# Optimization experiments

Measured on AMD Instinct MI355X. Metric: run time of the kernel, lower is better.

The kernel has to match this reference:

```python
import jax, jax.numpy as jnp
import numpy as np

B, T, D, H = 4096, 200, 128, 128


def setup_inputs() -> dict:
    key = jax.random.key(0)
    ks = jax.random.split(key, 9)
    s = 1.0 / np.sqrt(D + H)  # torch Linear default init bound
    u = lambda k, shape: jax.random.uniform(k, shape, jnp.float32, -s, s)
    return {
        "inputs": jax.random.normal(ks[0], (B, T, D), jnp.float32),
        "attention_scores": jax.random.uniform(ks[1], (B, T), jnp.float32),
        "h0": jnp.zeros((B, H), jnp.float32),
        "Wz": u(ks[2], (D + H, H)), "bz": u(ks[3], (H,)),
        "Wr": u(ks[4], (D + H, H)), "br": u(ks[5], (H,)),
        "Wh": u(ks[6], (D + H, H)), "bh": u(ks[7], (H,)),
    }


def reference(inputs, attention_scores, h0, Wz, bz, Wr, br, Wh, bh):
    # AUGRU: GRU with attention-modulated update gate (DIEN Sec 3.3).
    def step(h, xs):
        x_t, a_t = xs  # [B,D], [B]
        comb = jnp.concatenate([x_t, h], axis=-1)            # [B, D+H]
        z = jax.nn.sigmoid(comb @ Wz + bz)                   # [B, H]
        r = jax.nn.sigmoid(comb @ Wr + br)                   # [B, H]
        comb_r = jnp.concatenate([x_t, r * h], axis=-1)      # [B, D+H]
        h_tilde = jnp.tanh(comb_r @ Wh + bh)                 # [B, H]
        zp = a_t[:, None] * z                                # attention-scaled update gate
        h_new = (1.0 - zp) * h + zp * h_tilde
        return h_new, None

    xs = (jnp.swapaxes(inputs, 0, 1),            # [T, B, D]
          jnp.swapaxes(attention_scores, 0, 1))  # [T, B]
    h_final, _ = jax.lax.scan(step, h0, xs)
    return h_final  # [B, H]
```

## Files before the change

kernel.cpp:

```cpp
#include <hip/hip_runtime.h>
#include <stdint.h>

#define BB 4096
#define TT 200
#define DD 128
#define HH 128

typedef __attribute__((ext_vector_type(8))) short bf16x8;
typedef __attribute__((ext_vector_type(4))) float f32x4;

__device__ __forceinline__ short f2bf(float f) {
    uint32_t u = __builtin_bit_cast(uint32_t, f);
    u += 0x7fffu + ((u >> 16) & 1u);
    return (short)(u >> 16);
}
__device__ __forceinline__ uint32_t pk2(float a, float b) {
    uint32_t r;
    asm("v_cvt_pk_bf16_f32 %0, %1, %2" : "=v"(r) : "v"(a), "v"(b));
    return r;
}
__device__ __forceinline__ float sigm(float x) {
    return __builtin_amdgcn_rcpf(1.0f + __expf(-x));
}
__device__ __forceinline__ float tanhf_(float x) {
    return 2.0f * __builtin_amdgcn_rcpf(1.0f + __expf(-2.0f * x)) - 1.0f;
}
__device__ __forceinline__ void bar_lds() {
    asm volatile("s_waitcnt lgkmcnt(0)" ::: "memory");
    __builtin_amdgcn_sched_barrier(0);
    __builtin_amdgcn_s_barrier();
    __builtin_amdgcn_sched_barrier(0);
}


#define STEP(T, XR0, XR1) { \
    const int sn_ = ((T) + 1) & 1; \
    *(uint4*)&xbuf[sn_][xrow][xg_swz] = \
        make_uint4(pk2(XR0.x, XR0.y), pk2(XR0.z, XR0.w), \
                   pk2(XR1.x, XR1.y), pk2(XR1.z, XR1.w)); \
    { const int t3_ = ((T) + 3 < TT) ? (T) + 3 : TT - 1; \
      XR0 = *(const float4*)(xsrc + (size_t)t3_ * DD); \
      XR1 = *(const float4*)(xsrc + (size_t)t3_ * DD + 4); } \
    bf16x8 hf_[4]; \
    _Pragma("unroll") \
    for (int kt = 0; kt < 4; ++kt) hf_[kt] = hrow[fg[kt]]; \
    f32x4 az_[2], ar_[2]; \
    _Pragma("unroll") \
    for (int ct = 0; ct < 2; ++ct) { az_[ct] = pz[ct]; ar_[ct] = pr[ct]; } \
    _Pragma("unroll") \
    for (int kt = 0; kt < 4; ++kt) { \
        _Pragma("unroll") \
        for (int ct = 0; ct < 2; ++ct) { \
            az_[ct] = __builtin_amdgcn_mfma_f32_16x16x32_bf16(Wf[0][1][kt][ct], hf_[kt], az_[ct], 0, 0, 0); \
            ar_[ct] = __builtin_amdgcn_mfma_f32_16x16x32_bf16(Wf[1][1][kt][ct], hf_[kt], ar_[ct], 0, 0, 0); \
        } \
    } \
    f32x4 zv_[2], rhv_[2]; \
    _Pragma("unroll") \
    for (int ct = 0; ct < 2; ++ct) { \
        _Pragma("unroll") \
        for (int r = 0; r < 4; ++r) { \
            zv_[ct][r]  = sigm(az_[ct][r]); \
            rhv_[ct][r] = sigm(ar_[ct][r]) * hreg[ct][r]; \
        } \
        *(uint2*)((short*)&rhbuf[c][gout[ct]] + ohalf) = \
            make_uint2(pk2(rhv_[ct][0], rhv_[ct][1]), pk2(rhv_[ct][2], rhv_[ct][3])); \
    } \
    bar_lds(); \
    const float a_c_ = attbuf[c][(T)]; \
    bf16x8 rf_[4], xf2_[4]; \
    { const bf16x8* xp2_ = &xbuf[sn_][c][0]; \
      _Pragma("unroll") \
      for (int kt = 0; kt < 4; ++kt) { \
          rf_[kt]  = rhrow[fg[kt]]; \
          xf2_[kt] = xp2_[fg[kt]]; \
      } } \
    f32x4 ah_[2]; \
    _Pragma("unroll") \
    for (int ct = 0; ct < 2; ++ct) ah_[ct] = ph[ct]; \
    _Pragma("unroll") \
    for (int kt = 0; kt < 4; ++kt) { \
        _Pragma("unroll") \
        for (int ct = 0; ct < 2; ++ct) \
            ah_[ct] = __builtin_amdgcn_mfma_f32_16x16x32_bf16(Wf[2][1][kt][ct], rf_[kt], ah_[ct], 0, 0, 0); \
    } \
    _Pragma("unroll") \
    for (int ct = 0; ct < 2; ++ct) { pz[ct] = bzv[ct]; pr[ct] = brv[ct]; ph[ct] = bhv[ct]; } \
    _Pragma("unroll") \
    for (int kt = 0; kt < 4; ++kt) { \
        _Pragma("unroll") \
        for (int ct = 0; ct < 2; ++ct) { \
            pz[ct] = __builtin_amdgcn_mfma_f32_16x16x32_bf16(Wf[0][0][kt][ct], xf2_[kt], pz[ct], 0, 0, 0); \
            pr[ct] = __builtin_amdgcn_mfma_f32_16x16x32_bf16(Wf[1][0][kt][ct], xf2_[kt], pr[ct], 0, 0, 0); \
            ph[ct] = __builtin_amdgcn_mfma_f32_16x16x32_bf16(Wf[2][0][kt][ct], xf2_[kt], ph[ct], 0, 0, 0); \
        } \
    } \
    _Pragma("unroll") \
    for (int ct = 0; ct < 2; ++ct) { \
        _Pragma("unroll") \
        for (int r = 0; r < 4; ++r) { \
            float ht_ = tanhf_(ah_[ct][r]); \
            float zp_ = a_c_ * zv_[ct][r]; \
            hreg[ct][r] = __builtin_fmaf(zp_, ht_ - hreg[ct][r], hreg[ct][r]); \
        } \
        *(uint2*)((short*)&hbuf[c][gout[ct]] + ohalf) = \
            make_uint2(pk2(hreg[ct][0], hreg[ct][1]), pk2(hreg[ct][2], hreg[ct][3])); \
    } \
    bar_lds(); \
}

__global__ __launch_bounds__(256, 1) void augru_kernel(
    const float* __restrict__ inp,
    const float* __restrict__ att,
    const float* __restrict__ h0,
    const float* __restrict__ Wz, const float* __restrict__ bz,
    const float* __restrict__ Wr, const float* __restrict__ br,
    const float* __restrict__ Wh, const float* __restrict__ bh,
    float* __restrict__ out)
{
    __shared__ bf16x8 xbuf[2][16][16];
    __shared__ bf16x8 hbuf[16][16];
    __shared__ bf16x8 rhbuf[16][16];
    __shared__ float attbuf[16][201];

    const int tid  = threadIdx.x;
    const int wave = tid >> 6;
    const int lane = tid & 63;
    const int c    = lane & 15;
    const int grp  = lane >> 4;
    const int wbase = wave * 32;
    const int rowbase = blockIdx.x * 16;

    const int swz = c & 7;
    const int fg[4] = { (0 + grp) ^ swz, (4 + grp) ^ swz,
                        (8 + grp) ^ swz, (12 + grp) ^ swz };
    const int oc[2]   = { wbase + grp * 4, wbase + 16 + grp * 4 };
    const int gout[2] = { (4 * wave + (grp >> 1)) ^ swz,
                          (4 * wave + 2 + (grp >> 1)) ^ swz };
    const int ohalf = (grp & 1) * 4;
    const bf16x8* hrow  = &hbuf[c][0];
    const bf16x8* rhrow = &rhbuf[c][0];

    bf16x8 Wf[3][2][4][2];
    {
        const float* Wp[3] = {Wz, Wr, Wh};
        #pragma unroll
        for (int g3 = 0; g3 < 3; ++g3) {
            #pragma unroll
            for (int p = 0; p < 2; ++p) {
                #pragma unroll
                for (int kt = 0; kt < 4; ++kt) {
                    #pragma unroll
                    for (int ct = 0; ct < 2; ++ct) {
                        bf16x8 v;
                        #pragma unroll
                        for (int j = 0; j < 8; ++j) {
                            int k = p * 128 + kt * 32 + grp * 8 + j;
                            v[j] = f2bf(Wp[g3][(size_t)k * HH + wbase + ct * 16 + c]);
                        }
                        Wf[g3][p][kt][ct] = v;
                    }
                }
            }
        }
    }
    f32x4 bzv[2], brv[2], bhv[2];
    #pragma unroll
    for (int ct = 0; ct < 2; ++ct)
        #pragma unroll
        for (int r = 0; r < 4; ++r) {
            bzv[ct][r] = bz[oc[ct] + r];
            brv[ct][r] = br[oc[ct] + r];
            bhv[ct][r] = bh[oc[ct] + r];
        }

    for (int idx = tid; idx < 16 * TT; idx += 256)
        attbuf[idx / TT][idx % TT] = att[(size_t)rowbase * TT + idx];

    f32x4 hreg[2];
    #pragma unroll
    for (int ct = 0; ct < 2; ++ct) {
        float4 hv = *(const float4*)&h0[(size_t)(rowbase + c) * HH + oc[ct]];
        hreg[ct][0] = hv.x; hreg[ct][1] = hv.y; hreg[ct][2] = hv.z; hreg[ct][3] = hv.w;
        *(uint2*)((short*)&hbuf[c][gout[ct]] + ohalf) =
            make_uint2(pk2(hv.x, hv.y), pk2(hv.z, hv.w));
    }

    const int xrow = tid >> 4;
    const int xc8  = (tid & 15) * 8;
    const int xg_swz = (tid & 15) ^ (xrow & 7);
    const float* xsrc = inp + ((size_t)(rowbase + xrow) * TT) * DD + xc8;
    {
        float4 x0a = *(const float4*)(xsrc);
        float4 x0b = *(const float4*)(xsrc + 4);
        *(uint4*)&xbuf[0][xrow][xg_swz] =
            make_uint4(pk2(x0a.x, x0a.y), pk2(x0a.z, x0a.w),
                       pk2(x0b.x, x0b.y), pk2(x0b.z, x0b.w));
    }
    float4 xrA0 = *(const float4*)(xsrc + DD);
    float4 xrA1 = *(const float4*)(xsrc + DD + 4);
    float4 xrB0 = *(const float4*)(xsrc + 2 * DD);
    float4 xrB1 = *(const float4*)(xsrc + 2 * DD + 4);
    __syncthreads();

    f32x4 pz[2], pr[2], ph[2];
    #pragma unroll
    for (int ct = 0; ct < 2; ++ct) { pz[ct] = bzv[ct]; pr[ct] = brv[ct]; ph[ct] = bhv[ct]; }
    {
        const bf16x8* x0p = &xbuf[0][c][0];
        bf16x8 xf[4];
        #pragma unroll
        for (int kt = 0; kt < 4; ++kt) xf[kt] = x0p[fg[kt]];
        #pragma unroll
        for (int kt = 0; kt < 4; ++kt) {
            #pragma unroll
            for (int ct = 0; ct < 2; ++ct) {
                pz[ct] = __builtin_amdgcn_mfma_f32_16x16x32_bf16(Wf[0][0][kt][ct], xf[kt], pz[ct], 0, 0, 0);
                pr[ct] = __builtin_amdgcn_mfma_f32_16x16x32_bf16(Wf[1][0][kt][ct], xf[kt], pr[ct], 0, 0, 0);
                ph[ct] = __builtin_amdgcn_mfma_f32_16x16x32_bf16(Wf[2][0][kt][ct], xf[kt], ph[ct], 0, 0, 0);
            }
        }
    }

    for (int t = 0; t < TT; t += 2) {
        STEP(t, xrA0, xrA1);
        STEP(t + 1, xrB0, xrB1);
    }

    #pragma unroll
    for (int ct = 0; ct < 2; ++ct) {
        float4 o; o.x = hreg[ct][0]; o.y = hreg[ct][1]; o.z = hreg[ct][2]; o.w = hreg[ct][3];
        *(float4*)&out[(size_t)(rowbase + c) * HH + oc[ct]] = o;
    }
}

extern "C" void kernel_launch(void* const* d_in, const int* in_sizes, int n_in,
                              void* d_out, int out_size, void* d_ws, size_t ws_size,
                              hipStream_t stream) {
    const float* inp = (const float*)d_in[0];
    const float* att = (const float*)d_in[1];
    const float* h0  = (const float*)d_in[2];
    const float* Wz  = (const float*)d_in[3];
    const float* bz  = (const float*)d_in[4];
    const float* Wr  = (const float*)d_in[5];
    const float* br  = (const float*)d_in[6];
    const float* Wh  = (const float*)d_in[7];
    const float* bh  = (const float*)d_in[8];
    float* out = (float*)d_out;

    dim3 grid(BB / 16), block(256);
    augru_kernel<<<grid, block, 0, stream>>>(inp, att, h0, Wz, bz, Wr, br, Wh, bh, out);
}
```

Measured before the change: 216.8 us.

## Split recurrent MFMA chains into two accumulators and restage x prefetch

Each recurrent matmul's K-loop is split into two independent accumulator chains that are summed before the activations. This shortens the dependent MFMA chain on the serial per-step critical path. The x staging is also restructured: the x tile for step t+1 is loaded from LDS at the start of step t, the write into the double buffer moves after the gate computation, and the global prefetch distance grows to four steps. This adds extra adds and registers, plus an extra barrier in the prologue.

```diff
diff --git a/kernel.cpp b/kernel.cpp
--- a/kernel.cpp
+++ b/kernel.cpp
@@ -34,55 +34,67 @@
 
 
 #define STEP(T, XR0, XR1) { \
-    const int sn_ = ((T) + 1) & 1; \
-    *(uint4*)&xbuf[sn_][xrow][xg_swz] = \
+     \
+    bf16x8 hf_[4]; \
+    _Pragma("unroll") \
+    for (int kt = 0; kt < 4; ++kt) hf_[kt] = hrow[fg[kt]]; \
+    bf16x8 xf2_[4]; \
+    { const bf16x8* xp_ = &xbuf[((T) + 1) & 1][c][0]; \
+      _Pragma("unroll") \
+      for (int kt = 0; kt < 4; ++kt) xf2_[kt] = xp_[fg[kt]]; } \
+    const float a_c_ = attbuf[c][(T)]; \
+     \
+    f32x4 azA_[2], azB_[2], arA_[2], arB_[2]; \
+    _Pragma("unroll") \
+    for (int ct = 0; ct < 2; ++ct) { \
+        azA_[ct] = pz[ct]; arA_[ct] = pr[ct]; \
+        azB_[ct] = zzero;  arB_[ct] = zzero; \
+    } \
+    _Pragma("unroll") \
+    for (int kt = 0; kt < 2; ++kt) { \
+        _Pragma("unroll") \
+        for (int ct = 0; ct < 2; ++ct) { \
+            azA_[ct] = __builtin_amdgcn_mfma_f32_16x16x32_bf16(Wf[0][1][kt][ct], hf_[kt], azA_[ct], 0, 0, 0); \
+            arA_[ct] = __builtin_amdgcn_mfma_f32_16x16x32_bf16(Wf[1][1][kt][ct], hf_[kt], arA_[ct], 0, 0, 0); \
+            azB_[ct] = __builtin_amdgcn_mfma_f32_16x16x32_bf16(Wf[0][1][kt + 2][ct], hf_[kt + 2], azB_[ct], 0, 0, 0); \
+            arB_[ct] = __builtin_amdgcn_mfma_f32_16x16x32_bf16(Wf[1][1][kt + 2][ct], hf_[kt + 2], arB_[ct], 0, 0, 0); \
+        } \
+    } \
+    f32x4 zv_[2], rhv_[2]; \
+    _Pragma("unroll") \
+    for (int ct = 0; ct < 2; ++ct) { \
+        _Pragma("unroll") \
+        for (int r = 0; r < 4; ++r) { \
+            float az_ = azA_[ct][r] + azB_[ct][r]; \
+            float ar_ = arA_[ct][r] + arB_[ct][r]; \
+            zv_[ct][r]  = sigm(az_); \
+            rhv_[ct][r] = sigm(ar_) * hreg[ct][r]; \
+        } \
+        *(uint2*)((short*)&rhbuf[c][gout[ct]] + ohalf) = \
+            make_uint2(pk2(rhv_[ct][0], rhv_[ct][1]), pk2(rhv_[ct][2], rhv_[ct][3])); \
+    } \
+     \
+    *(uint4*)&xbuf[(T) & 1][xrow][xg_swz] = \
         make_uint4(pk2(XR0.x, XR0.y), pk2(XR0.z, XR0.w), \
                    pk2(XR1.x, XR1.y), pk2(XR1.z, XR1.w)); \
-    { const int t3_ = ((T) + 3 < TT) ? (T) + 3 : TT - 1; \
-      XR0 = *(const float4*)(xsrc + (size_t)t3_ * DD); \
-      XR1 = *(const float4*)(xsrc + (size_t)t3_ * DD + 4); } \
-    bf16x8 hf_[4]; \
-    _Pragma("unroll") \
-    for (int kt = 0; kt < 4; ++kt) hf_[kt] = hrow[fg[kt]]; \
-    f32x4 az_[2], ar_[2]; \
-    _Pragma("unroll") \
-    for (int ct = 0; ct < 2; ++ct) { az_[ct] = pz[ct]; ar_[ct] = pr[ct]; } \
-    _Pragma("unroll") \
-    for (int kt = 0; kt < 4; ++kt) { \
+    { const int t4_ = ((T) + 4 < TT) ? (T) + 4 : TT - 1; \
+      XR0 = *(const float4*)(xsrc + (size_t)t4_ * DD); \
+      XR1 = *(const float4*)(xsrc + (size_t)t4_ * DD + 4); } \
+    bar_lds(); \
+     \
+    bf16x8 rf_[4]; \
+    _Pragma("unroll") \
+    for (int kt = 0; kt < 4; ++kt) rf_[kt] = rhrow[fg[kt]]; \
+    f32x4 ahA_[2], ahB_[2]; \
+    _Pragma("unroll") \
+    for (int ct = 0; ct < 2; ++ct) { ahA_[ct] = ph[ct]; ahB_[ct] = zzero; } \
+    _Pragma("unroll") \
+    for (int kt = 0; kt < 2; ++kt) { \
         _Pragma("unroll") \
         for (int ct = 0; ct < 2; ++ct) { \
-            az_[ct] = __builtin_amdgcn_mfma_f32_16x16x32_bf16(Wf[0][1][kt][ct], hf_[kt], az_[ct], 0, 0, 0); \
-            ar_[ct] = __builtin_amdgcn_mfma_f32_16x16x32_bf16(Wf[1][1][kt][ct], hf_[kt], ar_[ct], 0, 0, 0); \
-        } \
-    } \
-    f32x4 zv_[2], rhv_[2]; \
-    _Pragma("unroll") \
-    for (int ct = 0; ct < 2; ++ct) { \
-        _Pragma("unroll") \
-        for (int r = 0; r < 4; ++r) { \
-            zv_[ct][r]  = sigm(az_[ct][r]); \
-            rhv_[ct][r] = sigm(ar_[ct][r]) * hreg[ct][r]; \
-        } \
-        *(uint2*)((short*)&rhbuf[c][gout[ct]] + ohalf) = \
-            make_uint2(pk2(rhv_[ct][0], rhv_[ct][1]), pk2(rhv_[ct][2], rhv_[ct][3])); \
-    } \
-    bar_lds(); \
-    const float a_c_ = attbuf[c][(T)]; \
-    bf16x8 rf_[4], xf2_[4]; \
-    { const bf16x8* xp2_ = &xbuf[sn_][c][0]; \
-      _Pragma("unroll") \
-      for (int kt = 0; kt < 4; ++kt) { \
-          rf_[kt]  = rhrow[fg[kt]]; \
-          xf2_[kt] = xp2_[fg[kt]]; \
-      } } \
-    f32x4 ah_[2]; \
-    _Pragma("unroll") \
-    for (int ct = 0; ct < 2; ++ct) ah_[ct] = ph[ct]; \
-    _Pragma("unroll") \
-    for (int kt = 0; kt < 4; ++kt) { \
-        _Pragma("unroll") \
-        for (int ct = 0; ct < 2; ++ct) \
-            ah_[ct] = __builtin_amdgcn_mfma_f32_16x16x32_bf16(Wf[2][1][kt][ct], rf_[kt], ah_[ct], 0, 0, 0); \
+            ahA_[ct] = __builtin_amdgcn_mfma_f32_16x16x32_bf16(Wf[2][1][kt][ct], rf_[kt], ahA_[ct], 0, 0, 0); \
+            ahB_[ct] = __builtin_amdgcn_mfma_f32_16x16x32_bf16(Wf[2][1][kt + 2][ct], rf_[kt + 2], ahB_[ct], 0, 0, 0); \
+        } \
     } \
     _Pragma("unroll") \
     for (int ct = 0; ct < 2; ++ct) { pz[ct] = bzv[ct]; pr[ct] = brv[ct]; ph[ct] = bhv[ct]; } \
@@ -99,7 +111,8 @@
     for (int ct = 0; ct < 2; ++ct) { \
         _Pragma("unroll") \
         for (int r = 0; r < 4; ++r) { \
-            float ht_ = tanhf_(ah_[ct][r]); \
+            float ah_ = ahA_[ct][r] + ahB_[ct][r]; \
+            float ht_ = tanhf_(ah_); \
             float zp_ = a_c_ * zv_[ct][r]; \
             hreg[ct][r] = __builtin_fmaf(zp_, ht_ - hreg[ct][r], hreg[ct][r]); \
         } \
@@ -130,6 +143,8 @@
     const int grp  = lane >> 4;
     const int wbase = wave * 32;
     const int rowbase = blockIdx.x * 16;
+
+    const f32x4 zzero = {0.0f, 0.0f, 0.0f, 0.0f};
 
     const int swz = c & 7;
     const int fg[4] = { (0 + grp) ^ swz, (4 + grp) ^ swz,
@@ -191,16 +206,21 @@
     const int xg_swz = (tid & 15) ^ (xrow & 7);
     const float* xsrc = inp + ((size_t)(rowbase + xrow) * TT) * DD + xc8;
     {
-        float4 x0a = *(const float4*)(xsrc);
-        float4 x0b = *(const float4*)(xsrc + 4);
+        float4 a0 = *(const float4*)(xsrc);
+        float4 a1 = *(const float4*)(xsrc + 4);
         *(uint4*)&xbuf[0][xrow][xg_swz] =
-            make_uint4(pk2(x0a.x, x0a.y), pk2(x0a.z, x0a.w),
-                       pk2(x0b.x, x0b.y), pk2(x0b.z, x0b.w));
-    }
-    float4 xrA0 = *(const float4*)(xsrc + DD);
-    float4 xrA1 = *(const float4*)(xsrc + DD + 4);
-    float4 xrB0 = *(const float4*)(xsrc + 2 * DD);
-    float4 xrB1 = *(const float4*)(xsrc + 2 * DD + 4);
+            make_uint4(pk2(a0.x, a0.y), pk2(a0.z, a0.w),
+                       pk2(a1.x, a1.y), pk2(a1.z, a1.w));
+        float4 b0 = *(const float4*)(xsrc + DD);
+        float4 b1 = *(const float4*)(xsrc + DD + 4);
+        *(uint4*)&xbuf[1][xrow][xg_swz] =
+            make_uint4(pk2(b0.x, b0.y), pk2(b0.z, b0.w),
+                       pk2(b1.x, b1.y), pk2(b1.z, b1.w));
+    }
+    float4 xrA0 = *(const float4*)(xsrc + 2 * DD);
+    float4 xrA1 = *(const float4*)(xsrc + 2 * DD + 4);
+    float4 xrB0 = *(const float4*)(xsrc + 3 * DD);
+    float4 xrB1 = *(const float4*)(xsrc + 3 * DD + 4);
     __syncthreads();
 
     f32x4 pz[2], pr[2], ph[2];
@@ -221,6 +241,7 @@
             }
         }
     }
+    __syncthreads();
 
     for (int t = 0; t < TT; t += 2) {
         STEP(t, xrA0, xrA1);
```

Result: slower. 227.6 us (+5.0%).
